# Performance work log

Measured on AMD Instinct MI355X. Metric: run time of the kernel, lower is better.

Reference implementation:

```python
import jax, jax.numpy as jnp
import numpy as np

B, N, F_IN, H, C, K = 32, 1024, 128, 64, 32, 2
L_HOP, NUM_ITER, TEMP = 2, 5, 0.5


def setup_inputs() -> dict:
    key = jax.random.key(0)
    ks = jax.random.split(key, 8)
    x = jax.random.normal(ks[0], (B, N, F_IN), jnp.float32)
    adj = jax.random.randint(ks[1], (B, N, N), 0, 2, jnp.int32)  # dense 0/1 adjacency per graph
    W_gcn = jax.random.normal(ks[2], (F_IN, H), jnp.float32) / np.sqrt(F_IN)
    b_gcn = jnp.zeros((H,), jnp.float32)
    W_unary = jax.random.normal(ks[3], (H, C), jnp.float32) / np.sqrt(H)
    b_unary = jnp.zeros((C,), jnp.float32)
    means = jax.random.normal(ks[4], (K, H), jnp.float32)
    scales = jnp.ones((K, H), jnp.float32) * 8.0  # widened so exp(-dist) stays in fp32 range
    kw = jnp.ones((K,), jnp.float32)
    mu = jax.random.normal(ks[5], (C, C), jnp.float32)
    return dict(x=x, adj=adj, W_gcn=W_gcn, b_gcn=b_gcn, W_unary=W_unary,
                b_unary=b_unary, means=means, scales=scales, kw=kw, mu=mu)


def _forward(x, adj_f, W_gcn, b_gcn, W_unary, b_unary, means, scales, kw, mu):
    n = x.shape[1]
    # --- GCN encode: D^{-1/2}(A+I)D^{-1/2} X W + b, relu ---
    a_hat = adj_f + jnp.eye(n, dtype=adj_f.dtype)
    dinv = jax.lax.rsqrt(a_hat.sum(-1))                       # [B,N], deg >= 1 via self-loop
    norm = dinv[:, :, None] * a_hat * dinv[:, None, :]        # [B,N,N]
    h = jax.nn.relu(jnp.einsum('bij,bjf,fh->bih', norm, x, W_gcn) + b_gcn)  # [B,N,H]
    # --- l-hop reachability mask ---
    adj_l = adj_f
    for _ in range(L_HOP - 1):
        adj_l = adj_l @ adj_f
    adj_l = (adj_l > 0).astype(h.dtype)                       # [B,N,N]
    # --- unary potentials ---
    unary = h @ W_unary + b_unary                             # [B,N,C]
    # --- Gaussian kernel: w_k * exp(dist_i[k] + dist_j[k]) == (e*w) @ e.T ---
    diff = (h[:, :, None, :] - means) / scales                # [B,N,K,H]
    e = jnp.exp(-jnp.sum(diff * diff, -1))                    # [B,N,K]
    pairwise = jnp.einsum('bik,k,bjk->bij', e, kw, e) * adj_l  # [B,N,N]
    # --- mean-field CRF iterations ---
    Q = jax.nn.softmax(unary, -1)
    for _ in range(NUM_ITER):
        msg = jnp.einsum('bij,bjc->bic', pairwise, Q @ mu)
        Q = jax.nn.softmax((unary + msg) / TEMP, -1)
    # --- soft-cluster pooling ---
    x_pooled = jnp.einsum('bnc,bnh->bch', Q, h)               # [B,C,H]
    adj_pooled = jnp.einsum('bnc,bnm,bmd->bcd', Q, adj_f, Q)  # [B,C,C]
    return x_pooled, adj_pooled


def reference(x, adj, W_gcn, b_gcn, W_unary, b_unary, means, scales, kw, mu):
    return _forward(x, adj.astype(x.dtype), W_gcn, b_gcn, W_unary, b_unary,
                    means, scales, kw, mu)
```

## Files before the change

### kernel.cpp

```cpp
#include <hip/hip_runtime.h>
#include <stdint.h>

#define NB  32
#define NN  1024
#define FIN 128
#define HH  64
#define CC  32
#define ZCAP 16
#define NITER 5

using short8  = __attribute__((ext_vector_type(8))) short;
using floatx4 = __attribute__((ext_vector_type(4))) float;

__device__ inline float b2f(unsigned short u) {
  union { uint32_t i; float f; } v; v.i = ((uint32_t)u) << 16; return v.f;
}
__device__ inline float b2f_lo(uint32_t w) {
  union { uint32_t i; float f; } v; v.i = w << 16; return v.f;
}
__device__ inline float b2f_hi(uint32_t w) {
  union { uint32_t i; float f; } v; v.i = w & 0xFFFF0000u; return v.f;
}
__device__ inline unsigned short f2b(float f) {
  union { uint32_t i; float f; } v; v.f = f;
  uint32_t r = v.i + 0x7FFFu + ((v.i >> 16) & 1u);
  return (unsigned short)(r >> 16);
}
__device__ inline floatx4 zf4() { floatx4 v = {0.f, 0.f, 0.f, 0.f}; return v; }

__global__ __launch_bounds__(256) void k_wcvt(const float* __restrict__ Wg,
    const float* __restrict__ Wu, unsigned short* __restrict__ Wgt,
    unsigned short* __restrict__ Wut, float* __restrict__ out, int out_n) {
  const int t = threadIdx.x;
  for (int idx = t; idx < HH * FIN; idx += 256) {
    int hh = idx >> 7, f = idx & 127;
    Wgt[idx] = f2b(Wg[f * HH + hh]);
  }
  for (int idx = t; idx < CC * HH; idx += 256) {
    int c = idx >> 6, f = idx & 63;
    Wut[idx] = f2b(Wu[f * CC + c]);
  }
  for (int idx = t; idx < out_n; idx += 256) out[idx] = 0.f;
}

__global__ __launch_bounds__(256) void k_bits(const int* __restrict__ adj,
    uint32_t* __restrict__ rowbits, float* __restrict__ dinv,
    int* __restrict__ zcnt) {
  __shared__ uint32_t rw[4][32];
  const int t = threadIdx.x, g = t >> 6, lane = t & 63;
  if (lane < 32) rw[g][lane] = 0u;
  __syncthreads();
  const size_t row = (size_t)blockIdx.x * 4 + g;
  int s = 0;
  #pragma unroll
  for (int rep = 0; rep < 4; rep++) {
    int4 a = ((const int4*)(adj + row * NN))[rep * 64 + lane];
    int b0 = (a.x != 0), b1 = (a.y != 0), b2 = (a.z != 0), b3 = (a.w != 0);
    uint32_t nib = ((uint32_t)(b0 | (b1 << 1) | (b2 << 2) | (b3 << 3))) << ((lane & 7) * 4);
    atomicOr(&rw[g][rep * 8 + (lane >> 3)], nib);
    s += b0 + b1 + b2 + b3;
  }
  #pragma unroll
  for (int m = 1; m < 64; m <<= 1) s += __shfl_xor(s, m, 64);
  __syncthreads();
  if (lane < 32) rowbits[row * 32 + lane] = rw[g][lane];
  if (lane == 0) { dinv[row] = rsqrtf((float)s + 1.0f); zcnt[row] = 0; }
}

__global__ __launch_bounds__(256) void k_cbits(const uint32_t* __restrict__ rowbits,
    uint32_t* __restrict__ colbits) {
  __shared__ uint32_t rbL[512 * 32];
  const int bid = blockIdx.x;
  const int b = bid >> 3, half = (bid >> 2) & 1, jt = bid & 3;
  const int t = threadIdx.x;
  const uint32_t* src = rowbits + ((size_t)b * NN + half * 512) * 32;
  for (int idx = t; idx < 512 * 32; idx += 256) rbL[idx] = src[idx];
  __syncthreads();
  const int j = jt * 256 + t, jw = j >> 5, jb = j & 31;
  uint32_t out[16];
  for (int w = 0; w < 16; w++) {
    uint32_t acc = 0;
    #pragma unroll
    for (int r = 0; r < 32; r++)
      acc |= ((rbL[(w * 32 + r) * 32 + jw] >> jb) & 1u) << r;
    out[w] = acc;
  }
  uint4* dst = (uint4*)(colbits + ((size_t)b * NN + j) * 32 + half * 16);
  #pragma unroll
  for (int x = 0; x < 4; x++) {
    uint4 v; v.x = out[4*x]; v.y = out[4*x+1]; v.z = out[4*x+2]; v.w = out[4*x+3];
    dst[x] = v;
  }
}

__global__ __launch_bounds__(256) void k_xw(const float* __restrict__ x,
    const unsigned short* __restrict__ Wgt, const float* __restrict__ dinv,
    unsigned short* __restrict__ xs, unsigned short* __restrict__ xst) {
  const int bid = blockIdx.x;
  const int b = bid >> 4;
  const int m0 = (bid & 15) * 64;
  const int t = threadIdx.x, wv = t >> 6, lane = t & 63, l15 = lane & 15, q = lane >> 4;
  const int mb = m0 + wv * 16;
  floatx4 acc[4];
  #pragma unroll
  for (int u = 0; u < 4; u++) acc[u] = zf4();
  #pragma unroll
  for (int k0 = 0; k0 < FIN; k0 += 32) {
    const float4* xp = (const float4*)(x + ((size_t)b * NN + mb + l15) * FIN + k0 + q * 8);
    float4 a0 = xp[0], a1 = xp[1];
    short8 af;
    af[0] = (short)f2b(a0.x); af[1] = (short)f2b(a0.y);
    af[2] = (short)f2b(a0.z); af[3] = (short)f2b(a0.w);
    af[4] = (short)f2b(a1.x); af[5] = (short)f2b(a1.y);
    af[6] = (short)f2b(a1.z); af[7] = (short)f2b(a1.w);
    #pragma unroll
    for (int u = 0; u < 4; u++) {
      short8 bf = *(const short8*)(Wgt + (u * 16 + l15) * FIN + k0 + q * 8);
      acc[u] = __builtin_amdgcn_mfma_f32_16x16x32_bf16(af, bf, acc[u], 0, 0, 0);
    }
  }
  #pragma unroll
  for (int r = 0; r < 4; r++) {
    const int i = mb + q * 4 + r;
    const float dv = dinv[b * NN + i];
    #pragma unroll
    for (int u = 0; u < 4; u++) {
      const int c = u * 16 + l15;
      unsigned short bv = f2b(dv * acc[u][r]);
      xs[((size_t)b * NN + i) * HH + c] = bv;
      xst[((size_t)b * HH + c) * NN + i] = bv;
    }
  }
}

__global__ __launch_bounds__(256) void k_gcnun(const uint32_t* __restrict__ rowbits,
    const unsigned short* __restrict__ xst, const unsigned short* __restrict__ xs,
    const float* __restrict__ dinv, const float* __restrict__ bg,
    const float* __restrict__ means, const float* __restrict__ scales,
    const unsigned short* __restrict__ Wut, const float* __restrict__ bu,
    float* __restrict__ h, float* __restrict__ e2, float* __restrict__ unary,
    unsigned short* __restrict__ Q0, float* __restrict__ Tp0) {
  __shared__ unsigned short hsh[4][16][72];
  __shared__ float Qs0[64][33];
  __shared__ float es0[64][2];
  const int bid = blockIdx.x;
  const int b = bid >> 4, blk = bid & 15;
  const int m0 = blk * 64;
  const int t = threadIdx.x, wv = t >> 6, lane = t & 63, l15 = lane & 15, q = lane >> 4;
  const int mb = m0 + wv * 16;
  floatx4 acc[4];
  #pragma unroll
  for (int u = 0; u < 4; u++) acc[u] = zf4();
  const uint32_t* rbrow = rowbits + ((size_t)b * NN + mb + l15) * 32;
  for (int k0 = 0; k0 < NN; k0 += 32) {
    uint32_t sh = rbrow[k0 >> 5] >> (q * 8);
    short8 af;
    #pragma unroll
    for (int jj = 0; jj < 8; jj++)
      af[jj] = (short)(((sh >> jj) & 1u) ? 0x3F80 : 0);
    #pragma unroll
    for (int u = 0; u < 4; u++) {
      short8 bf = *(const short8*)(xst + ((size_t)b * HH + u * 16 + l15) * NN + k0 + q * 8);
      acc[u] = __builtin_amdgcn_mfma_f32_16x16x32_bf16(af, bf, acc[u], 0, 0, 0);
    }
  }
  float bgc[4], mn0[4], mn1[4], is0[4], is1[4];
  #pragma unroll
  for (int u = 0; u < 4; u++) {
    const int c = u * 16 + l15;
    bgc[u] = bg[c];
    mn0[u] = means[c];        is0[u] = 1.0f / scales[c];
    mn1[u] = means[HH + c];   is1[u] = 1.0f / scales[HH + c];
  }
  #pragma unroll
  for (int r = 0; r < 4; r++) {
    const int i = mb + q * 4 + r;
    const float dv = dinv[b * NN + i];
    float dd0 = 0.f, dd1 = 0.f;
    #pragma unroll
    for (int u = 0; u < 4; u++) {
      const int c = u * 16 + l15;
      float xsv = b2f(xs[((size_t)b * NN + i) * HH + c]);
      float v = dv * (acc[u][r] + xsv) + bgc[u];
      v = v > 0.f ? v : 0.f;
      h[((size_t)b * NN + i) * HH + c] = v;
      unsigned short hb = f2b(v);
      hsh[wv][q * 4 + r][c] = hb;
      float vb = b2f(hb);
      float t0 = (vb - mn0[u]) * is0[u]; dd0 += t0 * t0;
      float t1 = (vb - mn1[u]) * is1[u]; dd1 += t1 * t1;
    }
    #pragma unroll
    for (int m = 1; m < 16; m <<= 1) {
      dd0 += __shfl_xor(dd0, m, 64);
      dd1 += __shfl_xor(dd1, m, 64);
    }
    if (l15 == 0) {
      float ev0 = __expf(-dd0), ev1 = __expf(-dd1);
      e2[((size_t)b * NN + i) * 2 + 0] = ev0;
      e2[((size_t)b * NN + i) * 2 + 1] = ev1;
      es0[wv * 16 + q * 4 + r][0] = ev0;
      es0[wv * 16 + q * 4 + r][1] = ev1;
    }
  }
  floatx4 uacc[2];
  uacc[0] = zf4(); uacc[1] = zf4();
  #pragma unroll
  for (int k0 = 0; k0 < HH; k0 += 32) {
    short8 af = *(const short8*)&hsh[wv][l15][k0 + q * 8];
    #pragma unroll
    for (int u = 0; u < 2; u++) {
      short8 bf = *(const short8*)(Wut + (u * 16 + l15) * HH + k0 + q * 8);
      uacc[u] = __builtin_amdgcn_mfma_f32_16x16x32_bf16(af, bf, uacc[u], 0, 0, 0);
    }
  }
  const float bu0 = bu[l15], bu1 = bu[16 + l15];
  #pragma unroll
  for (int r = 0; r < 4; r++) {
    const int i = mb + q * 4 + r;
    const int iloc = wv * 16 + q * 4 + r;
    float a0 = uacc[0][r] + bu0;
    float a1 = uacc[1][r] + bu1;
    unary[((size_t)b * NN + i) * CC + l15] = a0;
    unary[((size_t)b * NN + i) * CC + 16 + l15] = a1;
    float mx = fmaxf(a0, a1);
    #pragma unroll
    for (int m = 1; m < 16; m <<= 1) mx = fmaxf(mx, __shfl_xor(mx, m, 64));
    float x0 = __expf(a0 - mx), x1 = __expf(a1 - mx);
    float s = x0 + x1;
    #pragma unroll
    for (int m = 1; m < 16; m <<= 1) s += __shfl_xor(s, m, 64);
    float inv = 1.f / s;
    float q0v = x0 * inv, q1v = x1 * inv;
    Q0[((size_t)b * NN + i) * CC + l15] = f2b(q0v);
    Q0[((size_t)b * NN + i) * CC + 16 + l15] = f2b(q1v);
    Qs0[iloc][l15] = q0v;
    Qs0[iloc][16 + l15] = q1v;
  }
  __syncthreads();
  if (t < 64) {
    const int k = t >> 5, d = t & 31;
    float s = 0.f;
    #pragma unroll 8
    for (int i = 0; i < 64; i++) s += es0[i][k] * Qs0[i][d];
    Tp0[((size_t)b * 16 + blk) * 64 + t] = s;
  }
}

__global__ __launch_bounds__(256) void k_zscan(const uint32_t* __restrict__ rowbits,
    const uint32_t* __restrict__ colbits, int* __restrict__ zcnt,
    int* __restrict__ zidx) {
  __shared__ uint32_t rwL[128 * 32];
  const int bid = blockIdx.x;
  const int b = bid >> 3, it = bid & 7;
  const int i0 = it * 128;
  const int t = threadIdx.x;
  #pragma unroll
  for (int x = 0; x < 16; x++)
    rwL[x * 256 + t] = rowbits[((size_t)b * NN + i0) * 32 + x * 256 + t];
  __syncthreads();
  for (int jc = 0; jc < 4; jc++) {
    const int j = jc * 256 + t;
    uint32_t cb[32];
    const uint4* cbp = (const uint4*)(colbits + ((size_t)b * NN + j) * 32);
    #pragma unroll
    for (int x = 0; x < 8; x++) {
      uint4 v = cbp[x];
      cb[4*x] = v.x; cb[4*x+1] = v.y; cb[4*x+2] = v.z; cb[4*x+3] = v.w;
    }
    for (int i = 0; i < 128; i++) {
      uint32_t m = 0;
      for (int w = 0; w < 32; w++) {
        m |= rwL[i * 32 + w] & cb[w];
        if (__all(m != 0)) break;
      }
      if (m == 0) {
        int old = atomicAdd(&zcnt[b * NN + i0 + i], 1);
        if (old < ZCAP) zidx[(size_t)(b * NN + i0 + i) * ZCAP + old] = j;
      }
    }
  }
}

__global__ __launch_bounds__(256) void k_supd2(const float* __restrict__ unary,
    const float* __restrict__ e2g, const float* __restrict__ TpIn, int npart,
    const float* __restrict__ mu, const float* __restrict__ kwp,
    const int* __restrict__ zcnt, const int* __restrict__ zidx,
    const unsigned short* __restrict__ Qprev, unsigned short* __restrict__ Qnext,
    float* __restrict__ TpOut, const uint32_t* __restrict__ rowbits,
    const uint32_t* __restrict__ colbits, const float* __restrict__ h,
    unsigned short* __restrict__ qtb, float* __restrict__ out, int last) {
  __shared__ float muL[CC * CC];
  __shared__ float Tf[64];
  __shared__ float S[64];
  __shared__ uint32_t qs[256][17];
  __shared__ float es[256][2];
  __shared__ float part[4][64];
  const int bid = blockIdx.x;
  const int b = bid >> 2, seg = bid & 3;
  const int t = threadIdx.x;
  for (int i = t; i < CC * CC; i += 256) muL[i] = mu[i];
  if (t < 64) {
    float s = 0.f;
    for (int p = 0; p < npart; p++) s += TpIn[((size_t)b * npart + p) * 64 + t];
    Tf[t] = s;
  }
  __syncthreads();
  if (t < 64) {
    const int k = t >> 5, c = t & 31;
    float ss = 0.f;
    #pragma unroll 8
    for (int d = 0; d < CC; d++) ss += Tf[k * 32 + d] * muL[d * 32 + c];
    S[t] = ((k == 0) ? kwp[0] : kwp[1]) * ss;
  }
  __syncthreads();
  const int n = seg * 256 + t;
  const int gid = b * NN + n;
  const float e0 = e2g[(size_t)gid * 2 + 0];
  const float e1 = e2g[(size_t)gid * 2 + 1];
  es[t][0] = e0; es[t][1] = e1;
  float lg[CC];
  {
    const float4* ur = (const float4*)(unary + (size_t)gid * CC);
    const float4* S0 = (const float4*)S;
    const float4* S1 = (const float4*)(S + 32);
    #pragma unroll
    for (int c4 = 0; c4 < 8; c4++) {
      float4 uv = ur[c4], s0 = S0[c4], s1 = S1[c4];
      lg[c4*4]   = uv.x + e0 * s0.x + e1 * s1.x;
      lg[c4*4+1] = uv.y + e0 * s0.y + e1 * s1.y;
      lg[c4*4+2] = uv.z + e0 * s0.z + e1 * s1.z;
      lg[c4*4+3] = uv.w + e0 * s0.w + e1 * s1.w;
    }
  }
  const int zc = zcnt[gid];
  if (zc > 0) {
    const float kw0 = kwp[0], kw1 = kwp[1];
    if (zc <= ZCAP) {
      for (int z = 0; z < zc; z++) {
        const int j = zidx[(size_t)gid * ZCAP + z];
        const float w = kw0 * e0 * e2g[((size_t)b * NN + j) * 2 + 0]
                      + kw1 * e1 * e2g[((size_t)b * NN + j) * 2 + 1];
        const unsigned short* qj = Qprev + ((size_t)b * NN + j) * CC;
        for (int d = 0; d < CC; d++) {
          const float wq = w * b2f(qj[d]);
          #pragma unroll 8
          for (int c = 0; c < CC; c++) lg[c] -= wq * muL[d * CC + c];
        }
      }
    } else {
      const uint32_t* rbi = rowbits + (size_t)gid * 32;
      for (int j = 0; j < NN; j++) {
        uint32_t m = 0;
        const uint32_t* cbj = colbits + ((size_t)b * NN + j) * 32;
        for (int w32 = 0; w32 < 32; w32++) m |= rbi[w32] & cbj[w32];
        if (m == 0) {
          const float kw0b = kwp[0], kw1b = kwp[1];
          const float w = kw0b * e0 * e2g[((size_t)b * NN + j) * 2 + 0]
                        + kw1b * e1 * e2g[((size_t)b * NN + j) * 2 + 1];
          const unsigned short* qj = Qprev + ((size_t)b * NN + j) * CC;
          for (int d = 0; d < CC; d++) {
            const float wq = w * b2f(qj[d]);
            #pragma unroll 8
            for (int c = 0; c < CC; c++) lg[c] -= wq * muL[d * CC + c];
          }
        }
      }
    }
  }
  float mx = lg[0];
  #pragma unroll
  for (int c = 1; c < CC; c++) mx = fmaxf(mx, lg[c]);
  float ss = 0.f;
  #pragma unroll
  for (int c = 0; c < CC; c++) { lg[c] = __expf((lg[c] - mx) * 2.0f); ss += lg[c]; }
  const float inv = 1.f / ss;
  uint32_t pk[16];
  #pragma unroll
  for (int d2 = 0; d2 < 16; d2++) {
    pk[d2] = (uint32_t)f2b(lg[2*d2] * inv) | ((uint32_t)f2b(lg[2*d2+1] * inv) << 16);
    qs[t][d2] = pk[d2];
  }
  if (!last) {
    uint32_t* qn = (uint32_t*)(Qnext + (size_t)gid * CC);
    #pragma unroll
    for (int d2 = 0; d2 < 16; d2++) qn[d2] = pk[d2];
  }
  __syncthreads();
  if (!last) {
    const int kd = t & 63, d = t & 31, k = (t >> 5) & 1, sub = t >> 6;
    float s = 0.f;
    #pragma unroll 4
    for (int jj = 0; jj < 64; jj++) {
      const int j = sub * 64 + jj;
      const uint32_t w = qs[j][d >> 1];
      s += es[j][k] * ((d & 1) ? b2f_hi(w) : b2f_lo(w));
    }
    part[sub][kd] = s;
    __syncthreads();
    if (t < 64)
      TpOut[((size_t)b * 4 + seg) * 64 + t] = part[0][t] + part[1][t] + part[2][t] + part[3][t];
  } else {
    #pragma unroll
    for (int c = 0; c < CC; c++) {
      const uint32_t w = pk[c >> 1];
      qtb[((size_t)b * CC + c) * NN + n] =
          (unsigned short)((c & 1) ? (w >> 16) : (w & 0xFFFFu));
    }
    const int hh = t & 63, cg = t >> 6;
    float acc[8] = {0, 0, 0, 0, 0, 0, 0, 0};
    for (int jj = 0; jj < 256; jj++) {
      const int j = seg * 256 + jj;
      const float hv = h[((size_t)b * NN + j) * HH + hh];
      #pragma unroll
      for (int w = 0; w < 4; w++) {
        const uint32_t q2 = qs[jj][cg * 4 + w];
        acc[2*w]     += b2f_lo(q2) * hv;
        acc[2*w + 1] += b2f_hi(q2) * hv;
      }
    }
    #pragma unroll
    for (int k2 = 0; k2 < 8; k2++)
      atomicAdd(&out[((size_t)b * CC + cg * 8 + k2) * HH + hh], acc[k2]);
  }
}

__global__ __launch_bounds__(256) void k_adjqp(const uint32_t* __restrict__ rowbits,
    const unsigned short* __restrict__ qtb, float* __restrict__ out) {
  __shared__ float adjL[64][33];
  __shared__ float qL[64][32];
  const int bid = blockIdx.x;
  const int b = bid >> 4;
  const int m0 = (bid & 15) * 64;
  const int t = threadIdx.x, wv = t >> 6, lane = t & 63, l15 = lane & 15, q = lane >> 4;
  const int mb = m0 + wv * 16;
  floatx4 acc[2];
  acc[0] = zf4(); acc[1] = zf4();
  const uint32_t* rbrow = rowbits + ((size_t)b * NN + mb + l15) * 32;
  for (int k0 = 0; k0 < NN; k0 += 32) {
    uint32_t sh = rbrow[k0 >> 5] >> (q * 8);
    short8 af;
    #pragma unroll
    for (int jj = 0; jj < 8; jj++)
      af[jj] = (short)(((sh >> jj) & 1u) ? 0x3F80 : 0);
    #pragma unroll
    for (int u = 0; u < 2; u++) {
      short8 bf = *(const short8*)(qtb + ((size_t)b * CC + u * 16 + l15) * NN + k0 + q * 8);
      acc[u] = __builtin_amdgcn_mfma_f32_16x16x32_bf16(af, bf, acc[u], 0, 0, 0);
    }
  }
  #pragma unroll
  for (int r = 0; r < 4; r++)
    #pragma unroll
    for (int u = 0; u < 2; u++)
      adjL[wv * 16 + q * 4 + r][u * 16 + l15] = acc[u][r];
  #pragma unroll
  for (int x = 0; x < 8; x++) {
    const int idx = x * 256 + t;
    const int i = idx & 63, c = idx >> 6;
    qL[i][c] = b2f(qtb[((size_t)b * CC + c) * NN + m0 + i]);
  }
  __syncthreads();
  const int d = t & 31, cg = t >> 5;
  float a2[4] = {0, 0, 0, 0};
  for (int i = 0; i < 64; i++) {
    const float av = adjL[i][d];
    #pragma unroll
    for (int k = 0; k < 4; k++) a2[k] += qL[i][cg * 4 + k] * av;
  }
  #pragma unroll
  for (int k = 0; k < 4; k++)
    atomicAdd(&out[(size_t)NB * CC * HH + ((size_t)b * CC + cg * 4 + k) * CC + d], a2[k]);
}

extern "C" void kernel_launch(void* const* d_in, const int* in_sizes, int n_in,
                              void* d_out, int out_size, void* d_ws, size_t ws_size,
                              hipStream_t stream) {
  (void)in_sizes; (void)n_in; (void)out_size;
  const float* x      = (const float*)d_in[0];
  const int*   adj    = (const int*)d_in[1];
  const float* Wg     = (const float*)d_in[2];
  const float* bg     = (const float*)d_in[3];
  const float* Wu     = (const float*)d_in[4];
  const float* bu     = (const float*)d_in[5];
  const float* means  = (const float*)d_in[6];
  const float* scales = (const float*)d_in[7];
  const float* kw     = (const float*)d_in[8];
  const float* mu     = (const float*)d_in[9];

  char* ws = (char*)d_ws;
  size_t off = 0;
  auto alloc = [&](size_t bytes) { char* p = ws + off; off += (bytes + 255) & ~(size_t)255; return p; };
  uint32_t*       rbits = (uint32_t*)alloc((size_t)NB * NN * 32 * 4);
  uint32_t*       cbits = (uint32_t*)alloc((size_t)NB * NN * 32 * 4);
  float*          dinv  = (float*)alloc((size_t)NB * NN * 4);
  unsigned short* Wgt   = (unsigned short*)alloc((size_t)HH * FIN * 2);
  unsigned short* Wut   = (unsigned short*)alloc((size_t)CC * HH * 2);
  unsigned short* xs    = (unsigned short*)alloc((size_t)NB * NN * HH * 2);
  unsigned short* xst   = (unsigned short*)alloc((size_t)NB * HH * NN * 2);
  float*          h     = (float*)alloc((size_t)NB * NN * HH * 4);
  float*          e2    = (float*)alloc((size_t)NB * NN * 2 * 4);
  float*          unary = (float*)alloc((size_t)NB * NN * CC * 4);
  int*            zcnt  = (int*)alloc((size_t)NB * NN * 4);
  int*            zidx  = (int*)alloc((size_t)NB * NN * ZCAP * 4);
  unsigned short* Qa    = (unsigned short*)alloc((size_t)NB * NN * CC * 2);
  unsigned short* Qb    = (unsigned short*)alloc((size_t)NB * NN * CC * 2);
  unsigned short* qtb   = (unsigned short*)alloc((size_t)NB * CC * NN * 2);
  float*          Tp0   = (float*)alloc((size_t)NB * 16 * 64 * 4);
  float*          TpA   = (float*)alloc((size_t)NB * 4 * 64 * 4);
  float*          TpB   = (float*)alloc((size_t)NB * 4 * 64 * 4);
  if (off > ws_size) return;

  float* out = (float*)d_out;
  const int out_n = NB * CC * (HH + CC);

  k_wcvt <<<1, 256, 0, stream>>>(Wg, Wu, Wgt, Wut, out, out_n);
  k_bits <<<NB * NN / 4, 256, 0, stream>>>(adj, rbits, dinv, zcnt);
  k_cbits<<<NB * 8, 256, 0, stream>>>(rbits, cbits);
  k_zscan<<<NB * 8, 256, 0, stream>>>(rbits, cbits, zcnt, zidx);
  k_xw   <<<NB * 16, 256, 0, stream>>>(x, Wgt, dinv, xs, xst);
  k_gcnun<<<NB * 16, 256, 0, stream>>>(rbits, xst, xs, dinv, bg, means, scales,
                                       Wut, bu, h, e2, unary, Qa, Tp0);
  unsigned short* qprev = Qa; unsigned short* qnext = Qb;
  const float* tin = Tp0; int npart = 16; float* tout = TpA;
  for (int it = 0; it < NITER; it++) {
    const int last = (it == NITER - 1) ? 1 : 0;
    k_supd2<<<NB * 4, 256, 0, stream>>>(unary, e2, tin, npart, mu, kw, zcnt, zidx,
                                        qprev, qnext, tout, rbits, cbits, h,
                                        qtb, out, last);
    unsigned short* tmpq = qprev; qprev = qnext; qnext = tmpq;
    tin = tout; npart = 4;
    tout = (tout == TpA) ? TpB : TpA;
  }
  k_adjqp<<<NB * 16, 256, 0, stream>>>(rbits, qtb, out);
}
```

Baseline: 419.1 us.

## Compute 2-hop zero mask via neighbor row OR, drop column-bit transpose

Replaces the column-bitmask transpose and the row-by-column AND scan with a per-row union of neighbor rows' bitmasks, exiting early once all bits are set. This finds the unreachable (i,j) pairs without building colbits. The zero scan is merged into the XW GEMM kernel as extra blocks, and the weight conversion is folded into the bits kernel, cutting launches from five to two. The overflow fallback in the CRF update now walks neighbor rows instead of reading colbits, which may be slower when that path is hit.

```diff
diff --git a/kernel.cpp b/kernel.cpp
--- a/kernel.cpp
+++ b/kernel.cpp
@@ -28,26 +28,26 @@
 }
 __device__ inline floatx4 zf4() { floatx4 v = {0.f, 0.f, 0.f, 0.f}; return v; }
 
-__global__ __launch_bounds__(256) void k_wcvt(const float* __restrict__ Wg,
+__global__ __launch_bounds__(256) void k_bits(const int* __restrict__ adj,
+    uint32_t* __restrict__ rowbits, float* __restrict__ dinv,
+    int* __restrict__ zcnt, const float* __restrict__ Wg,
     const float* __restrict__ Wu, unsigned short* __restrict__ Wgt,
     unsigned short* __restrict__ Wut, float* __restrict__ out, int out_n) {
   const int t = threadIdx.x;
-  for (int idx = t; idx < HH * FIN; idx += 256) {
-    int hh = idx >> 7, f = idx & 127;
-    Wgt[idx] = f2b(Wg[f * HH + hh]);
-  }
-  for (int idx = t; idx < CC * HH; idx += 256) {
-    int c = idx >> 6, f = idx & 63;
-    Wut[idx] = f2b(Wu[f * CC + c]);
-  }
-  for (int idx = t; idx < out_n; idx += 256) out[idx] = 0.f;
-}
-
-__global__ __launch_bounds__(256) void k_bits(const int* __restrict__ adj,
-    uint32_t* __restrict__ rowbits, float* __restrict__ dinv,
-    int* __restrict__ zcnt) {
+  if (blockIdx.x == NB * NN / 4) {
+    for (int idx = t; idx < HH * FIN; idx += 256) {
+      int hh = idx >> 7, f = idx & 127;
+      Wgt[idx] = f2b(Wg[f * HH + hh]);
+    }
+    for (int idx = t; idx < CC * HH; idx += 256) {
+      int c = idx >> 6, f = idx & 63;
+      Wut[idx] = f2b(Wu[f * CC + c]);
+    }
+    for (int idx = t; idx < out_n; idx += 256) out[idx] = 0.f;
+    return;
+  }
   __shared__ uint32_t rw[4][32];
-  const int t = threadIdx.x, g = t >> 6, lane = t & 63;
+  const int g = t >> 6, lane = t & 63;
   if (lane < 32) rw[g][lane] = 0u;
   __syncthreads();
   const size_t row = (size_t)blockIdx.x * 4 + g;
@@ -67,39 +67,48 @@
   if (lane == 0) { dinv[row] = rsqrtf((float)s + 1.0f); zcnt[row] = 0; }
 }
 
-__global__ __launch_bounds__(256) void k_cbits(const uint32_t* __restrict__ rowbits,
-    uint32_t* __restrict__ colbits) {
-  __shared__ uint32_t rbL[512 * 32];
-  const int bid = blockIdx.x;
-  const int b = bid >> 3, half = (bid >> 2) & 1, jt = bid & 3;
+__global__ __launch_bounds__(256) void k_xwz(const float* __restrict__ x,
+    const unsigned short* __restrict__ Wgt, const float* __restrict__ dinv,
+    unsigned short* __restrict__ xs, unsigned short* __restrict__ xst,
+    const uint32_t* __restrict__ rowbits, int* __restrict__ zcnt,
+    int* __restrict__ zidx) {
   const int t = threadIdx.x;
-  const uint32_t* src = rowbits + ((size_t)b * NN + half * 512) * 32;
-  for (int idx = t; idx < 512 * 32; idx += 256) rbL[idx] = src[idx];
-  __syncthreads();
-  const int j = jt * 256 + t, jw = j >> 5, jb = j & 31;
-  uint32_t out[16];
-  for (int w = 0; w < 16; w++) {
-    uint32_t acc = 0;
-    #pragma unroll
-    for (int r = 0; r < 32; r++)
-      acc |= ((rbL[(w * 32 + r) * 32 + jw] >> jb) & 1u) << r;
-    out[w] = acc;
-  }
-  uint4* dst = (uint4*)(colbits + ((size_t)b * NN + j) * 32 + half * 16);
-  #pragma unroll
-  for (int x = 0; x < 4; x++) {
-    uint4 v; v.x = out[4*x]; v.y = out[4*x+1]; v.z = out[4*x+2]; v.w = out[4*x+3];
-    dst[x] = v;
-  }
-}
-
-__global__ __launch_bounds__(256) void k_xw(const float* __restrict__ x,
-    const unsigned short* __restrict__ Wgt, const float* __restrict__ dinv,
-    unsigned short* __restrict__ xs, unsigned short* __restrict__ xst) {
+  if (blockIdx.x >= NB * 16) {
+    const int zbid = blockIdx.x - NB * 16;
+    const int b = zbid >> 4, i0 = (zbid & 15) * 64;
+    const int wv = t >> 6, lane = t & 63, lw = lane & 31;
+    for (int rep = 0; rep < 16; rep++) {
+      const int i = i0 + wv * 16 + rep;
+      const uint32_t* rbi = rowbits + ((size_t)b * NN + i) * 32;
+      uint32_t u = 0;
+      int done = 0;
+      for (int wi = 0; wi < 32 && !done; wi++) {
+        uint32_t wb = rbi[wi];
+        while (wb) {
+          const int p = __ffs(wb) - 1;
+          wb &= wb - 1;
+          const int k = wi * 32 + p;
+          u |= rowbits[((size_t)b * NN + k) * 32 + lw];
+          if (__all(u == 0xFFFFFFFFu)) { done = 1; break; }
+        }
+      }
+      if (!done && lane < 32) {
+        uint32_t miss = ~u;
+        while (miss) {
+          const int p = __ffs(miss) - 1;
+          miss &= miss - 1;
+          const int j = lw * 32 + p;
+          int old = atomicAdd(&zcnt[b * NN + i], 1);
+          if (old < ZCAP) zidx[(size_t)(b * NN + i) * ZCAP + old] = j;
+        }
+      }
+    }
+    return;
+  }
   const int bid = blockIdx.x;
   const int b = bid >> 4;
   const int m0 = (bid & 15) * 64;
-  const int t = threadIdx.x, wv = t >> 6, lane = t & 63, l15 = lane & 15, q = lane >> 4;
+  const int wv = t >> 6, lane = t & 63, l15 = lane & 15, q = lane >> 4;
   const int mb = m0 + wv * 16;
   floatx4 acc[4];
   #pragma unroll
@@ -247,49 +256,14 @@
   }
 }
 
-__global__ __launch_bounds__(256) void k_zscan(const uint32_t* __restrict__ rowbits,
-    const uint32_t* __restrict__ colbits, int* __restrict__ zcnt,
-    int* __restrict__ zidx) {
-  __shared__ uint32_t rwL[128 * 32];
-  const int bid = blockIdx.x;
-  const int b = bid >> 3, it = bid & 7;
-  const int i0 = it * 128;
-  const int t = threadIdx.x;
-  #pragma unroll
-  for (int x = 0; x < 16; x++)
-    rwL[x * 256 + t] = rowbits[((size_t)b * NN + i0) * 32 + x * 256 + t];
-  __syncthreads();
-  for (int jc = 0; jc < 4; jc++) {
-    const int j = jc * 256 + t;
-    uint32_t cb[32];
-    const uint4* cbp = (const uint4*)(colbits + ((size_t)b * NN + j) * 32);
-    #pragma unroll
-    for (int x = 0; x < 8; x++) {
-      uint4 v = cbp[x];
-      cb[4*x] = v.x; cb[4*x+1] = v.y; cb[4*x+2] = v.z; cb[4*x+3] = v.w;
-    }
-    for (int i = 0; i < 128; i++) {
-      uint32_t m = 0;
-      for (int w = 0; w < 32; w++) {
-        m |= rwL[i * 32 + w] & cb[w];
-        if (__all(m != 0)) break;
-      }
-      if (m == 0) {
-        int old = atomicAdd(&zcnt[b * NN + i0 + i], 1);
-        if (old < ZCAP) zidx[(size_t)(b * NN + i0 + i) * ZCAP + old] = j;
-      }
-    }
-  }
-}
-
 __global__ __launch_bounds__(256) void k_supd2(const float* __restrict__ unary,
     const float* __restrict__ e2g, const float* __restrict__ TpIn, int npart,
     const float* __restrict__ mu, const float* __restrict__ kwp,
     const int* __restrict__ zcnt, const int* __restrict__ zidx,
     const unsigned short* __restrict__ Qprev, unsigned short* __restrict__ Qnext,
     float* __restrict__ TpOut, const uint32_t* __restrict__ rowbits,
-    const uint32_t* __restrict__ colbits, const float* __restrict__ h,
-    unsigned short* __restrict__ qtb, float* __restrict__ out, int last) {
+    const float* __restrict__ h, unsigned short* __restrict__ qtb,
+    float* __restrict__ out, int last) {
   __shared__ float muL[CC * CC];
   __shared__ float Tf[64];
   __shared__ float S[64];
@@ -351,13 +325,21 @@
     } else {
       const uint32_t* rbi = rowbits + (size_t)gid * 32;
       for (int j = 0; j < NN; j++) {
-        uint32_t m = 0;
-        const uint32_t* cbj = colbits + ((size_t)b * NN + j) * 32;
-        for (int w32 = 0; w32 < 32; w32++) m |= rbi[w32] & cbj[w32];
-        if (m == 0) {
-          const float kw0b = kwp[0], kw1b = kwp[1];
-          const float w = kw0b * e0 * e2g[((size_t)b * NN + j) * 2 + 0]
-                        + kw1b * e1 * e2g[((size_t)b * NN + j) * 2 + 1];
+        int found = 0;
+        for (int wi = 0; wi < 32 && !found; wi++) {
+          uint32_t wb = rbi[wi];
+          while (wb) {
+            const int p = __ffs(wb) - 1;
+            wb &= wb - 1;
+            const int k = wi * 32 + p;
+            if ((rowbits[((size_t)b * NN + k) * 32 + (j >> 5)] >> (j & 31)) & 1u) {
+              found = 1; break;
+            }
+          }
+        }
+        if (!found) {
+          const float w = kw0 * e0 * e2g[((size_t)b * NN + j) * 2 + 0]
+                        + kw1 * e1 * e2g[((size_t)b * NN + j) * 2 + 1];
           const unsigned short* qj = Qprev + ((size_t)b * NN + j) * CC;
           for (int d = 0; d < CC; d++) {
             const float wq = w * b2f(qj[d]);
@@ -492,7 +474,6 @@
   size_t off = 0;
   auto alloc = [&](size_t bytes) { char* p = ws + off; off += (bytes + 255) & ~(size_t)255; return p; };
   uint32_t*       rbits = (uint32_t*)alloc((size_t)NB * NN * 32 * 4);
-  uint32_t*       cbits = (uint32_t*)alloc((size_t)NB * NN * 32 * 4);
   float*          dinv  = (float*)alloc((size_t)NB * NN * 4);
   unsigned short* Wgt   = (unsigned short*)alloc((size_t)HH * FIN * 2);
   unsigned short* Wut   = (unsigned short*)alloc((size_t)CC * HH * 2);
@@ -514,11 +495,9 @@
   float* out = (float*)d_out;
   const int out_n = NB * CC * (HH + CC);
 
-  k_wcvt <<<1, 256, 0, stream>>>(Wg, Wu, Wgt, Wut, out, out_n);
-  k_bits <<<NB * NN / 4, 256, 0, stream>>>(adj, rbits, dinv, zcnt);
-  k_cbits<<<NB * 8, 256, 0, stream>>>(rbits, cbits);
-  k_zscan<<<NB * 8, 256, 0, stream>>>(rbits, cbits, zcnt, zidx);
-  k_xw   <<<NB * 16, 256, 0, stream>>>(x, Wgt, dinv, xs, xst);
+  k_bits <<<NB * NN / 4 + 1, 256, 0, stream>>>(adj, rbits, dinv, zcnt,
+                                               Wg, Wu, Wgt, Wut, out, out_n);
+  k_xwz  <<<NB * 32, 256, 0, stream>>>(x, Wgt, dinv, xs, xst, rbits, zcnt, zidx);
   k_gcnun<<<NB * 16, 256, 0, stream>>>(rbits, xst, xs, dinv, bg, means, scales,
                                        Wut, bu, h, e2, unary, Qa, Tp0);
   unsigned short* qprev = Qa; unsigned short* qnext = Qb;
@@ -526,8 +505,7 @@
   for (int it = 0; it < NITER; it++) {
     const int last = (it == NITER - 1) ? 1 : 0;
     k_supd2<<<NB * 4, 256, 0, stream>>>(unary, e2, tin, npart, mu, kw, zcnt, zidx,
-                                        qprev, qnext, tout, rbits, cbits, h,
-                                        qtb, out, last);
+                                        qprev, qnext, tout, rbits, h, qtb, out, last);
     unsigned short* tmpq = qprev; qprev = qnext; qnext = tmpq;
     tin = tout; npart = 4;
     tout = (tout == TpA) ? TpB : TpA;
```

After: 394.7 us (median of 2 runs). 1.06x faster.
